# Performance work log

Measured on AMD Instinct MI355X. Metric: run time of the kernel, lower is better.

The kernel has to match this reference:

```python
import jax, jax.numpy as jnp
import numpy as np

NUM_RELATIONS = 8


def rgcn_conv(x, edge_index, edge_type, W, root, bias):
    """PyG-style RGCNConv with mean aggregation per relation.
    x: [N, Fin], edge_index: [2, E], edge_type: [E],
    W: [R, Fin, Fout], root: [Fin, Fout], bias: [Fout].
    """
    src, dst = edge_index[0], edge_index[1]
    N = x.shape[0]
    out = x @ root + bias  # root/self transform
    for r in range(NUM_RELATIONS):
        mask = (edge_type == r)
        h = x @ W[r]  # transform nodes first: [N, Fout] (cheaper than per-edge)
        msg = jnp.where(mask[:, None], h[src], jnp.zeros((), x.dtype))  # [E, Fout]
        agg = jax.ops.segment_sum(msg, dst, num_segments=N)  # [N, Fout]
        cnt = jax.ops.segment_sum(mask.astype(x.dtype), dst, num_segments=N)
        out = out + agg / jnp.maximum(cnt, 1.0)[:, None]  # mean per relation
    return out


def setup_inputs() -> dict:
    key = jax.random.key(0)
    ks = jax.random.split(key, 16)
    N, E, Fin, H, R = 100000, 600000, 128, 128, NUM_RELATIONS
    x = jax.random.normal(ks[0], (N, Fin), dtype=jnp.float32)
    edge_index = jax.random.randint(ks[1], (2, E), 0, N, dtype=jnp.int64)
    edge_type = jax.random.randint(ks[2], (E,), 0, R, dtype=jnp.int64)
    s = 0.05
    return {
        "x": x,
        "edge_index": edge_index,
        "edge_type": edge_type,
        "W1": jax.random.normal(ks[3], (R, Fin, H), dtype=jnp.float32) * s,
        "root1": jax.random.normal(ks[4], (Fin, H), dtype=jnp.float32) * s,
        "b1": jnp.zeros((H,), dtype=jnp.float32),
        "W2": jax.random.normal(ks[5], (R, H, H), dtype=jnp.float32) * s,
        "root2": jax.random.normal(ks[6], (H, H), dtype=jnp.float32) * s,
        "b2": jnp.zeros((H,), dtype=jnp.float32),
        "W3": jax.random.normal(ks[7], (R, H, H), dtype=jnp.float32) * s,
        "root3": jax.random.normal(ks[8], (H, H), dtype=jnp.float32) * s,
        "b3": jnp.zeros((H,), dtype=jnp.float32),
    }


def reference(x, edge_index, edge_type, W1, root1, b1, W2, root2, b2, W3, root3, b3):
    h = jax.nn.relu(rgcn_conv(x, edge_index, edge_type, W1, root1, b1))
    h = jax.nn.relu(rgcn_conv(h, edge_index, edge_type, W2, root2, b2))
    h = jax.nn.relu(rgcn_conv(h, edge_index, edge_type, W3, root3, b3))
    return h
```

## Files before the change

kernel.cpp:

```cpp
#include <hip/hip_runtime.h>

#define FDIM 128
#define NREL 8
#define SCHUNK 4096

typedef __attribute__((ext_vector_type(8))) short bf16x8;
typedef __attribute__((ext_vector_type(8))) unsigned short u16x8;
typedef __attribute__((ext_vector_type(4))) float f32x4;

__device__ __forceinline__ unsigned short f2bf(float f) {
  unsigned int u = __float_as_uint(f);
  u += 0x7fffu + ((u >> 16) & 1u);
  return (unsigned short)(u >> 16);
}


__global__ void zero_u32(unsigned int* __restrict__ p, long n) {
  long i = (long)blockIdx.x * blockDim.x + threadIdx.x;
  long s = (long)gridDim.x * blockDim.x;
  for (; i < n; i += s) p[i] = 0u;
}

__global__ void hist_k(const int* __restrict__ dst, const int* __restrict__ et,
                       int E, int* __restrict__ cnt, int N) {
  int e = blockIdx.x * 256 + threadIdx.x;
  if (e < E) atomicAdd(&cnt[et[e] * N + dst[e]], 1);
}

__global__ void scan_partial(const int* __restrict__ cnt, int n, int* __restrict__ sums) {
  __shared__ int red[256];
  int base = blockIdx.x * SCHUNK;
  int s = 0;
  for (int i = threadIdx.x; i < SCHUNK; i += 256) {
    int j = base + i;
    s += (j < n) ? cnt[j] : 0;
  }
  red[threadIdx.x] = s;
  __syncthreads();
  for (int o = 128; o > 0; o >>= 1) {
    if (threadIdx.x < o) red[threadIdx.x] += red[threadIdx.x + o];
    __syncthreads();
  }
  if (threadIdx.x == 0) sums[blockIdx.x] = red[0];
}

__global__ void scan_sums(int* __restrict__ sums, int nb) {
  __shared__ int tmp[256];
  int t = threadIdx.x;
  int v = (t < nb) ? sums[t] : 0;
  tmp[t] = v;
  __syncthreads();
  for (int o = 1; o < 256; o <<= 1) {
    int u = (t >= o) ? tmp[t - o] : 0;
    __syncthreads();
    tmp[t] += u;
    __syncthreads();
  }
  if (t < nb) sums[t] = tmp[t] - v;
}

__global__ void scan_final(const int* __restrict__ cnt, int n,
                           const int* __restrict__ sums, int* __restrict__ off) {
  __shared__ int red[256];
  int t = threadIdx.x;
  int base = blockIdx.x * SCHUNK;
  int loc[16];
  int s = 0;
#pragma unroll
  for (int i = 0; i < 16; ++i) {
    int j = base + t * 16 + i;
    int v = (j < n) ? cnt[j] : 0;
    loc[i] = s;
    s += v;
  }
  red[t] = s;
  __syncthreads();
  int mine = s;
  for (int o = 1; o < 256; o <<= 1) {
    int u = (t >= o) ? red[t - o] : 0;
    __syncthreads();
    red[t] += u;
    __syncthreads();
  }
  int tp = red[t] - mine;
  int bb = sums[blockIdx.x];
#pragma unroll
  for (int i = 0; i < 16; ++i) {
    int j = base + t * 16 + i;
    if (j < n) off[j] = bb + tp + loc[i];
  }
}

__global__ void sort_k(const int* __restrict__ src, const int* __restrict__ dst,
                       const int* __restrict__ et, int E, int* __restrict__ cur,
                       int* __restrict__ ss, int N) {
  int e = blockIdx.x * 256 + threadIdx.x;
  if (e < E) {
    int key = et[e] * N + dst[e];
    int p = atomicAdd(&cur[key], 1);
    ss[p] = src[e];
  }
}

__global__ void wtrans_k(const float* __restrict__ r1, const float* __restrict__ w1,
                         const float* __restrict__ r2, const float* __restrict__ w2,
                         const float* __restrict__ r3, const float* __restrict__ w3,
                         unsigned short* __restrict__ Wt) {
  int b = blockIdx.x;
  int L = b / 9, s = b % 9;
  const float* root = (L == 0) ? r1 : (L == 1) ? r2 : r3;
  const float* W = (L == 0) ? w1 : (L == 1) ? w2 : w3;
  const float* src = (s == 0) ? root : W + (size_t)(s - 1) * FDIM * FDIM;
  unsigned short* out = Wt + (size_t)b * FDIM * FDIM;
  for (int i = threadIdx.x; i < FDIM * FDIM; i += 256) {
    int j = i >> 7, k = i & 127;
    out[i] = f2bf(src[k * FDIM + j]);
  }
}

__global__ void seg_mean_k(const float* __restrict__ x, const int* __restrict__ ss,
                           const int* __restrict__ off, int key0, int nkeys,
                           unsigned short* __restrict__ pre) {
  int g = blockIdx.x * 8 + (threadIdx.x >> 5);
  if (g >= nkeys) return;
  int lane = threadIdx.x & 31;
  int s = off[key0 + g], e = off[key0 + g + 1];
  float4 a = make_float4(0.f, 0.f, 0.f, 0.f);
  for (int i = s; i < e; ++i) {
    const float4 v = ((const float4*)(x + (size_t)ss[i] * FDIM))[lane];
    a.x += v.x; a.y += v.y; a.z += v.z; a.w += v.w;
  }
  float sc = (e > s) ? 1.0f / (float)(e - s) : 0.f;
  ushort4 o;
  o.x = f2bf(a.x * sc); o.y = f2bf(a.y * sc);
  o.z = f2bf(a.z * sc); o.w = f2bf(a.w * sc);
  ((ushort4*)(pre + (size_t)g * FDIM))[lane] = o;
}

__global__ __launch_bounds__(256) void layer_gemm(
    const float* __restrict__ A0, const unsigned short* __restrict__ pre,
    const unsigned short* __restrict__ Wt, const float* __restrict__ bias,
    float* __restrict__ C, int N, int n_pre, int do_relu) {
  __shared__ __align__(16) unsigned short As[FDIM * FDIM];
  __shared__ __align__(16) unsigned short Bs[FDIM * FDIM];
  const int tid = threadIdx.x;
  const int row0 = blockIdx.x * 128;
  const int wave = tid >> 6, lane = tid & 63;
  const int l16 = lane & 15, lq = lane >> 4;
  const int do_init = (A0 != nullptr);

  f32x4 acc[2][8];
#pragma unroll
  for (int m = 0; m < 2; ++m)
#pragma unroll
    for (int n = 0; n < 8; ++n) acc[m][n] = (f32x4){0.f, 0.f, 0.f, 0.f};

  const int n_src = n_pre + do_init;
  for (int s = 0; s < n_src; ++s) {
    __syncthreads();
    {
      const u16x8* g = (const u16x8*)(Wt + (size_t)s * FDIM * FDIM);
#pragma unroll
      for (int i = 0; i < 8; ++i) {
        int u = tid + 256 * i;
        int r = u >> 4, kb = u & 15;
        ((u16x8*)Bs)[(r << 4) | (kb ^ (r & 7))] = g[u];
      }
    }
    if (do_init && s == 0) {
#pragma unroll
      for (int i = 0; i < 8; ++i) {
        int u = tid + 256 * i;
        int r = u >> 4, kb = u & 15;
        int grow = row0 + r;
        u16x8 v = {0, 0, 0, 0, 0, 0, 0, 0};
        if (grow < N) {
          const float4* rp = (const float4*)(A0 + (size_t)grow * FDIM);
          float4 f0 = rp[kb * 2], f1 = rp[kb * 2 + 1];
          v = (u16x8){f2bf(f0.x), f2bf(f0.y), f2bf(f0.z), f2bf(f0.w),
                      f2bf(f1.x), f2bf(f1.y), f2bf(f1.z), f2bf(f1.w)};
        }
        ((u16x8*)As)[(r << 4) | (kb ^ (r & 7))] = v;
      }
    } else {
      const unsigned short* base = pre + (size_t)(s - do_init) * N * FDIM;
#pragma unroll
      for (int i = 0; i < 8; ++i) {
        int u = tid + 256 * i;
        int r = u >> 4, kb = u & 15;
        int grow = row0 + r;
        u16x8 v = {0, 0, 0, 0, 0, 0, 0, 0};
        if (grow < N) v = ((const u16x8*)(base + (size_t)grow * FDIM))[kb];
        ((u16x8*)As)[(r << 4) | (kb ^ (r & 7))] = v;
      }
    }
    __syncthreads();
#pragma unroll
    for (int kk = 0; kk < 4; ++kk) {
      bf16x8 a[2], b[8];
#pragma unroll
      for (int m = 0; m < 2; ++m) {
        int r = wave * 32 + m * 16 + l16;
        a[m] = ((const bf16x8*)As)[(r << 4) | ((kk * 4 + lq) ^ (r & 7))];
      }
#pragma unroll
      for (int n = 0; n < 8; ++n) {
        int r = n * 16 + l16;
        b[n] = ((const bf16x8*)Bs)[(r << 4) | ((kk * 4 + lq) ^ (r & 7))];
      }
#pragma unroll
      for (int m = 0; m < 2; ++m)
#pragma unroll
        for (int n = 0; n < 8; ++n)
          acc[m][n] = __builtin_amdgcn_mfma_f32_16x16x32_bf16(a[m], b[n], acc[m][n], 0, 0, 0);
    }
  }

#pragma unroll
  for (int m = 0; m < 2; ++m) {
    int rbase = row0 + wave * 32 + m * 16 + lq * 4;
#pragma unroll
    for (int n = 0; n < 8; ++n) {
      int col = (n << 4) | l16;
#pragma unroll
      for (int r = 0; r < 4; ++r) {
        int row = rbase + r;
        if (row < N) {
          size_t idx = (size_t)row * FDIM + col;
          float v = acc[m][n][r];
          v += do_init ? bias[col] : C[idx];
          if (do_relu) v = fmaxf(v, 0.f);
          C[idx] = v;
        }
      }
    }
  }
}


extern "C" void kernel_launch(void* const* d_in, const int* in_sizes, int n_in,
                              void* d_out, int out_size, void* d_ws, size_t ws_size,
                              hipStream_t stream) {
  const float* x = (const float*)d_in[0];
  const int* ei = (const int*)d_in[1];
  const int* et = (const int*)d_in[2];
  const float* W[3]    = {(const float*)d_in[3], (const float*)d_in[6], (const float*)d_in[9]};
  const float* root[3] = {(const float*)d_in[4], (const float*)d_in[7], (const float*)d_in[10]};
  const float* bias[3] = {(const float*)d_in[5], (const float*)d_in[8], (const float*)d_in[11]};

  const int N = in_sizes[0] / FDIM;
  const int E = in_sizes[1] / 2;
  const int* src = ei;
  const int* dst = ei + E;
  const int NK = NREL * N;

  char* w = (char*)d_ws;
  size_t pos = 0;
  auto carve = [&](size_t bytes) -> void* {
    pos = (pos + 255) & ~(size_t)255;
    void* p = w + pos;
    pos += bytes;
    return p;
  };
  int* cnt = (int*)carve(sizeof(int) * (NK + 1));
  int* off = (int*)carve(sizeof(int) * (NK + 1));
  int* cur = (int*)carve(sizeof(int) * (NK + 1));
  int* sums = (int*)carve(sizeof(int) * 512);
  int* ss = (int*)carve(sizeof(int) * E);
  unsigned short* Wt = (unsigned short*)carve(sizeof(unsigned short) * 27 * FDIM * FDIM);
  float* h1 = (float*)carve(sizeof(float) * (size_t)N * FDIM);
  float* h2 = (float*)carve(sizeof(float) * (size_t)N * FDIM);
  size_t fixed = (pos + 255) & ~(size_t)255;
  int G = NREL;
  while (G > 1 && fixed + sizeof(unsigned short) * (size_t)G * N * FDIM > ws_size) G >>= 1;
  unsigned short* pre = (unsigned short*)carve(sizeof(unsigned short) * (size_t)G * N * FDIM);

  zero_u32<<<1024, 256, 0, stream>>>((unsigned int*)cnt, NK + 1);
  hist_k<<<(E + 255) / 256, 256, 0, stream>>>(dst, et, E, cnt, N);
  const int n_scan = NK + 1;
  const int nchunk = (n_scan + SCHUNK - 1) / SCHUNK;
  scan_partial<<<nchunk, 256, 0, stream>>>(cnt, n_scan, sums);
  scan_sums<<<1, 256, 0, stream>>>(sums, nchunk);
  scan_final<<<nchunk, 256, 0, stream>>>(cnt, n_scan, sums, off);
  hipMemcpyAsync(cur, off, sizeof(int) * NK, hipMemcpyDeviceToDevice, stream);
  sort_k<<<(E + 255) / 256, 256, 0, stream>>>(src, dst, et, E, cur, ss, N);
  wtrans_k<<<27, 256, 0, stream>>>(root[0], W[0], root[1], W[1], root[2], W[2], Wt);

  const float* in_p = x;
  float* outs[3] = {h1, h2, (float*)d_out};
  const int npass = NREL / G;
  for (int L = 0; L < 3; ++L) {
    unsigned short* WtL = Wt + (size_t)L * 9 * FDIM * FDIM;
    for (int p = 0; p < npass; ++p) {
      seg_mean_k<<<(G * N) / 8, 256, 0, stream>>>(in_p, ss, off, p * G * N, G * N, pre);
      const unsigned short* Wpass = WtL + (size_t)(p == 0 ? 0 : 1 + p * G) * FDIM * FDIM;
      layer_gemm<<<(N + 127) / 128, 256, 0, stream>>>(
          p == 0 ? in_p : nullptr, pre, Wpass, bias[L], outs[L], N, G,
          (p == npass - 1) ? 1 : 0);
    }
    in_p = outs[L];
  }
}
```

Before: 837.7 us.

## Fuse per-relation segment mean into GEMM using LDS atomic accumulation

Replaces the separate seg_mean kernel (which wrote bf16 per-relation means to a large global buffer) and the layer GEMM with one fused kernel per layer. Each 64-row block gathers source rows for its destination nodes per relation, accumulates them into LDS with float atomics, scales by the inverse count, and feeds the result straight into MFMA. Weight tiles are prefetched into registers for the next relation. The sorted edge list now also stores the destination. This removes the global round trip of the intermediate and the extra launches, at the cost of LDS atomic contention, halved GEMM rows per block, and serialised gather and compute phases inside the block.

After: 1.756 ms. 2.1x slower.

```diff
diff --git a/kernel.cpp b/kernel.cpp
--- a/kernel.cpp
+++ b/kernel.cpp
@@ -2,6 +2,7 @@
 
 #define FDIM 128
 #define NREL 8
+#define BM 64
 #define SCHUNK 4096
 
 typedef __attribute__((ext_vector_type(8))) short bf16x8;
@@ -93,12 +94,13 @@
 
 __global__ void sort_k(const int* __restrict__ src, const int* __restrict__ dst,
                        const int* __restrict__ et, int E, int* __restrict__ cur,
-                       int* __restrict__ ss, int N) {
+                       int2* __restrict__ ssd, int N) {
   int e = blockIdx.x * 256 + threadIdx.x;
   if (e < E) {
-    int key = et[e] * N + dst[e];
+    int d = dst[e];
+    int key = et[e] * N + d;
     int p = atomicAdd(&cur[key], 1);
-    ss[p] = src[e];
+    ssd[p] = make_int2(src[e], d);
   }
 }
 
@@ -118,121 +120,133 @@
   }
 }
 
-__global__ void seg_mean_k(const float* __restrict__ x, const int* __restrict__ ss,
-                           const int* __restrict__ off, int key0, int nkeys,
-                           unsigned short* __restrict__ pre) {
-  int g = blockIdx.x * 8 + (threadIdx.x >> 5);
-  if (g >= nkeys) return;
-  int lane = threadIdx.x & 31;
-  int s = off[key0 + g], e = off[key0 + g + 1];
-  float4 a = make_float4(0.f, 0.f, 0.f, 0.f);
-  for (int i = s; i < e; ++i) {
-    const float4 v = ((const float4*)(x + (size_t)ss[i] * FDIM))[lane];
-    a.x += v.x; a.y += v.y; a.z += v.z; a.w += v.w;
-  }
-  float sc = (e > s) ? 1.0f / (float)(e - s) : 0.f;
-  ushort4 o;
-  o.x = f2bf(a.x * sc); o.y = f2bf(a.y * sc);
-  o.z = f2bf(a.z * sc); o.w = f2bf(a.w * sc);
-  ((ushort4*)(pre + (size_t)g * FDIM))[lane] = o;
-}
-
-__global__ __launch_bounds__(256) void layer_gemm(
-    const float* __restrict__ A0, const unsigned short* __restrict__ pre,
-    const unsigned short* __restrict__ Wt, const float* __restrict__ bias,
-    float* __restrict__ C, int N, int n_pre, int do_relu) {
-  __shared__ __align__(16) unsigned short As[FDIM * FDIM];
+__global__ __launch_bounds__(256) void fused_layer(
+    const float* __restrict__ in, const int2* __restrict__ ssd,
+    const int* __restrict__ off, const unsigned short* __restrict__ Wt,
+    const float* __restrict__ bias, float* __restrict__ out, int N) {
+  __shared__ __align__(16) float accs[BM * FDIM];
   __shared__ __align__(16) unsigned short Bs[FDIM * FDIM];
+  __shared__ float scl[BM];
+
   const int tid = threadIdx.x;
-  const int row0 = blockIdx.x * 128;
   const int wave = tid >> 6, lane = tid & 63;
   const int l16 = lane & 15, lq = lane >> 4;
-  const int do_init = (A0 != nullptr);
-
-  f32x4 acc[2][8];
-#pragma unroll
-  for (int m = 0; m < 2; ++m)
-#pragma unroll
-    for (int n = 0; n < 8; ++n) acc[m][n] = (f32x4){0.f, 0.f, 0.f, 0.f};
-
-  const int n_src = n_pre + do_init;
-  for (int s = 0; s < n_src; ++s) {
-    __syncthreads();
-    {
-      const u16x8* g = (const u16x8*)(Wt + (size_t)s * FDIM * FDIM);
+  const int c4 = tid & 31, grp = tid >> 5;
+  const int row0 = blockIdx.x * BM;
+  const int nrows = min(BM, N - row0);
+
+  f32x4 pacc[8];
+#pragma unroll
+  for (int n = 0; n < 8; ++n) pacc[n] = (f32x4){0.f, 0.f, 0.f, 0.f};
+
+  u16x8 breg[8];
+  {
+    const u16x8* g = (const u16x8*)Wt;
+#pragma unroll
+    for (int i = 0; i < 8; ++i) breg[i] = g[tid + 256 * i];
+  }
+
+  for (int s = 0; s < 1 + NREL; ++s) {
+    __syncthreads();
+
+#pragma unroll
+    for (int i = 0; i < 8; ++i) {
+      int u = tid + 256 * i;
+      int r = u >> 4, kb = u & 15;
+      ((u16x8*)Bs)[(r << 4) | (kb ^ (r & 7))] = breg[i];
+    }
+    if (s > 0) {
+#pragma unroll
+      for (int i = 0; i < 8; ++i)
+        ((float4*)accs)[tid + 256 * i] = make_float4(0.f, 0.f, 0.f, 0.f);
+    }
+    if (s < NREL) {
+      const u16x8* g = (const u16x8*)(Wt + (size_t)(s + 1) * FDIM * FDIM);
+#pragma unroll
+      for (int i = 0; i < 8; ++i) breg[i] = g[tid + 256 * i];
+    }
+    __syncthreads();
+
+    if (s == 0) {
 #pragma unroll
       for (int i = 0; i < 8; ++i) {
         int u = tid + 256 * i;
-        int r = u >> 4, kb = u & 15;
-        ((u16x8*)Bs)[(r << 4) | (kb ^ (r & 7))] = g[u];
-      }
-    }
-    if (do_init && s == 0) {
-#pragma unroll
-      for (int i = 0; i < 8; ++i) {
-        int u = tid + 256 * i;
-        int r = u >> 4, kb = u & 15;
-        int grow = row0 + r;
-        u16x8 v = {0, 0, 0, 0, 0, 0, 0, 0};
-        if (grow < N) {
-          const float4* rp = (const float4*)(A0 + (size_t)grow * FDIM);
-          float4 f0 = rp[kb * 2], f1 = rp[kb * 2 + 1];
-          v = (u16x8){f2bf(f0.x), f2bf(f0.y), f2bf(f0.z), f2bf(f0.w),
-                      f2bf(f1.x), f2bf(f1.y), f2bf(f1.z), f2bf(f1.w)};
+        int r = u >> 5, c = u & 31;
+        float4 v = make_float4(0.f, 0.f, 0.f, 0.f);
+        if (r < nrows) v = ((const float4*)(in + (size_t)(row0 + r) * FDIM))[c];
+        ((float4*)accs)[(r << 5) | (c ^ (r & 7))] = v;
+      }
+    } else {
+      const int rel = s - 1;
+      const int key0 = rel * N + row0;
+      if (tid < BM) {
+        float sc = 0.f;
+        if (tid < nrows) {
+          int c = off[key0 + tid + 1] - off[key0 + tid];
+          sc = (c > 0) ? 1.0f / (float)c : 0.f;
         }
-        ((u16x8*)As)[(r << 4) | (kb ^ (r & 7))] = v;
-      }
-    } else {
-      const unsigned short* base = pre + (size_t)(s - do_init) * N * FDIM;
-#pragma unroll
-      for (int i = 0; i < 8; ++i) {
-        int u = tid + 256 * i;
-        int r = u >> 4, kb = u & 15;
-        int grow = row0 + r;
-        u16x8 v = {0, 0, 0, 0, 0, 0, 0, 0};
-        if (grow < N) v = ((const u16x8*)(base + (size_t)grow * FDIM))[kb];
-        ((u16x8*)As)[(r << 4) | (kb ^ (r & 7))] = v;
-      }
-    }
-    __syncthreads();
+        scl[tid] = sc;
+      }
+      const int ebase = off[key0];
+      const int eend = off[key0 + nrows];
+      int e = ebase + grp;
+      int2 ed;
+      float4 v;
+      bool have = (e < eend);
+      if (have) {
+        ed = ssd[e];
+        v = ((const float4*)(in + (size_t)ed.x * FDIM))[c4];
+      }
+      while (have) {
+        int e2 = e + 8;
+        int2 ed2;
+        float4 v2;
+        bool have2 = (e2 < eend);
+        if (have2) {
+          ed2 = ssd[e2];
+          v2 = ((const float4*)(in + (size_t)ed2.x * FDIM))[c4];
+        }
+        int lr = ed.y - row0;
+        float* ap = &accs[(((lr << 5) | (c4 ^ (lr & 7))) << 2)];
+        atomicAdd(ap + 0, v.x);
+        atomicAdd(ap + 1, v.y);
+        atomicAdd(ap + 2, v.z);
+        atomicAdd(ap + 3, v.w);
+        e = e2; ed = ed2; v = v2; have = have2;
+      }
+    }
+    __syncthreads();
+
+    const int arow = wave * 16 + l16;
+    const float sc = (s == 0) ? 1.0f : scl[arow];
 #pragma unroll
     for (int kk = 0; kk < 4; ++kk) {
-      bf16x8 a[2], b[8];
-#pragma unroll
-      for (int m = 0; m < 2; ++m) {
-        int r = wave * 32 + m * 16 + l16;
-        a[m] = ((const bf16x8*)As)[(r << 4) | ((kk * 4 + lq) ^ (r & 7))];
-      }
+      int cu = (kk * 4 + lq) * 2;
+      f32x4 f0 = ((const f32x4*)accs)[(arow << 5) | (cu ^ (arow & 7))];
+      f32x4 f1 = ((const f32x4*)accs)[(arow << 5) | ((cu + 1) ^ (arow & 7))];
+      bf16x8 a;
+      a[0] = (short)f2bf(f0[0] * sc); a[1] = (short)f2bf(f0[1] * sc);
+      a[2] = (short)f2bf(f0[2] * sc); a[3] = (short)f2bf(f0[3] * sc);
+      a[4] = (short)f2bf(f1[0] * sc); a[5] = (short)f2bf(f1[1] * sc);
+      a[6] = (short)f2bf(f1[2] * sc); a[7] = (short)f2bf(f1[3] * sc);
 #pragma unroll
       for (int n = 0; n < 8; ++n) {
-        int r = n * 16 + l16;
-        b[n] = ((const bf16x8*)Bs)[(r << 4) | ((kk * 4 + lq) ^ (r & 7))];
-      }
-#pragma unroll
-      for (int m = 0; m < 2; ++m)
-#pragma unroll
-        for (int n = 0; n < 8; ++n)
-          acc[m][n] = __builtin_amdgcn_mfma_f32_16x16x32_bf16(a[m], b[n], acc[m][n], 0, 0, 0);
-    }
-  }
-
-#pragma unroll
-  for (int m = 0; m < 2; ++m) {
-    int rbase = row0 + wave * 32 + m * 16 + lq * 4;
-#pragma unroll
-    for (int n = 0; n < 8; ++n) {
-      int col = (n << 4) | l16;
-#pragma unroll
-      for (int r = 0; r < 4; ++r) {
-        int row = rbase + r;
-        if (row < N) {
-          size_t idx = (size_t)row * FDIM + col;
-          float v = acc[m][n][r];
-          v += do_init ? bias[col] : C[idx];
-          if (do_relu) v = fmaxf(v, 0.f);
-          C[idx] = v;
-        }
-      }
+        int br = n * 16 + l16;
+        bf16x8 b = ((const bf16x8*)Bs)[(br << 4) | ((kk * 4 + lq) ^ (br & 7))];
+        pacc[n] = __builtin_amdgcn_mfma_f32_16x16x32_bf16(a, b, pacc[n], 0, 0, 0);
+      }
+    }
+  }
+
+#pragma unroll
+  for (int n = 0; n < 8; ++n) {
+    int col = (n << 4) | l16;
+    float bv = bias[col];
+#pragma unroll
+    for (int rr = 0; rr < 4; ++rr) {
+      int row = wave * 16 + lq * 4 + rr;
+      if (row0 + row < N)
+        out[(size_t)(row0 + row) * FDIM + col] = fmaxf(pacc[n][rr] + bv, 0.f);
     }
   }
 }
@@ -266,14 +280,10 @@
   int* off = (int*)carve(sizeof(int) * (NK + 1));
   int* cur = (int*)carve(sizeof(int) * (NK + 1));
   int* sums = (int*)carve(sizeof(int) * 512);
-  int* ss = (int*)carve(sizeof(int) * E);
+  int2* ssd = (int2*)carve(sizeof(int2) * E);
   unsigned short* Wt = (unsigned short*)carve(sizeof(unsigned short) * 27 * FDIM * FDIM);
   float* h1 = (float*)carve(sizeof(float) * (size_t)N * FDIM);
   float* h2 = (float*)carve(sizeof(float) * (size_t)N * FDIM);
-  size_t fixed = (pos + 255) & ~(size_t)255;
-  int G = NREL;
-  while (G > 1 && fixed + sizeof(unsigned short) * (size_t)G * N * FDIM > ws_size) G >>= 1;
-  unsigned short* pre = (unsigned short*)carve(sizeof(unsigned short) * (size_t)G * N * FDIM);
 
   zero_u32<<<1024, 256, 0, stream>>>((unsigned int*)cnt, NK + 1);
   hist_k<<<(E + 255) / 256, 256, 0, stream>>>(dst, et, E, cnt, N);
@@ -283,21 +293,15 @@
   scan_sums<<<1, 256, 0, stream>>>(sums, nchunk);
   scan_final<<<nchunk, 256, 0, stream>>>(cnt, n_scan, sums, off);
   hipMemcpyAsync(cur, off, sizeof(int) * NK, hipMemcpyDeviceToDevice, stream);
-  sort_k<<<(E + 255) / 256, 256, 0, stream>>>(src, dst, et, E, cur, ss, N);
+  sort_k<<<(E + 255) / 256, 256, 0, stream>>>(src, dst, et, E, cur, ssd, N);
   wtrans_k<<<27, 256, 0, stream>>>(root[0], W[0], root[1], W[1], root[2], W[2], Wt);
 
+  const int NB = (N + BM - 1) / BM;
   const float* in_p = x;
   float* outs[3] = {h1, h2, (float*)d_out};
-  const int npass = NREL / G;
   for (int L = 0; L < 3; ++L) {
-    unsigned short* WtL = Wt + (size_t)L * 9 * FDIM * FDIM;
-    for (int p = 0; p < npass; ++p) {
-      seg_mean_k<<<(G * N) / 8, 256, 0, stream>>>(in_p, ss, off, p * G * N, G * N, pre);
-      const unsigned short* Wpass = WtL + (size_t)(p == 0 ? 0 : 1 + p * G) * FDIM * FDIM;
-      layer_gemm<<<(N + 127) / 128, 256, 0, stream>>>(
-          p == 0 ? in_p : nullptr, pre, Wpass, bias[L], outs[L], N, G,
-          (p == npass - 1) ? 1 : 0);
-    }
+    const unsigned short* WtL = Wt + (size_t)L * 9 * FDIM * FDIM;
+    fused_layer<<<NB, 256, 0, stream>>>(in_p, ssd, off, WtL, bias[L], outs[L], N);
     in_p = outs[L];
   }
 }
```
